# Optimization experiments

Hardware: AMD Instinct MI355X
Metric: run time of the kernel (lower is better)

Reference implementation:

```python
import jax, jax.numpy as jnp
import numpy as np

N, F, F_, H = 8192, 1024, 64, 4
LEAKY_ALPHA = 0.2
MASK_VAL = -1e10


def setup_inputs() -> dict:
    key = jax.random.key(0)
    k1, k2, k3, k4 = jax.random.split(key, 4)
    X = jax.random.normal(k1, (N, F), dtype=jnp.float32)
    # sparse-ish binary adjacency with self loops (A = A + I in the source script)
    A = (jax.random.uniform(k2, (N, N)) < 0.004).astype(jnp.float32)
    A = jnp.clip(A + jnp.eye(N, dtype=jnp.float32), 0.0, 1.0)
    W = jax.random.normal(k3, (H, F, F_), dtype=jnp.float32) * (1.0 / np.sqrt(F))
    attn_a = jax.random.normal(k4, (H, 2 * F_, 1), dtype=jnp.float32) * (1.0 / np.sqrt(2 * F_))
    bias = jnp.zeros((H, F_), dtype=jnp.float32)
    return {"X": X, "A": A, "W": W, "attn_a": attn_a, "bias": bias}


def reference(X, A, W, attn_a, bias):
    # features per head: [H, N, F_]
    feats = jnp.einsum('nf,hfk->hnk', X, W)
    # concat-score trick: [f_i, f_j] @ a == f_i @ a[:F_] + f_j @ a[F_:]
    a_self = attn_a[:, :F_, 0]   # [H, F_]
    a_neigh = attn_a[:, F_:, 0]  # [H, F_]
    s_self = jnp.einsum('hnk,hk->hn', feats, a_self)   # [H, N]
    s_neigh = jnp.einsum('hnk,hk->hn', feats, a_neigh)  # [H, N]
    scores = s_self[:, :, None] + s_neigh[:, None, :]   # [H, N, N]
    scores = jnp.where(scores > 0, scores, LEAKY_ALPHA * scores)  # LeakyReLU(0.2)
    scores = scores + MASK_VAL * (1.0 - A)[None]
    attn = jax.nn.softmax(scores, axis=-1)              # [H, N, N]
    # aggregate (dropout is identity at inference)
    out = jnp.einsum('hij,hjk->hik', attn, feats) + bias[:, None, :]  # [H, N, F_]
    out = jnp.transpose(out, (1, 0, 2)).reshape(X.shape[0], H * F_)   # concat heads
    return jax.nn.relu(out)
```

## Files before the change

kernel.cpp:

```cpp
#include <hip/hip_runtime.h>
#include <hip/hip_bf16.h>
#include <stdint.h>

#define NN 8192
#define FF 1024
#define FD 64
#define NH 4
#define CC 256
#define MAXE 192

typedef __attribute__((ext_vector_type(8))) short short8;
typedef __attribute__((ext_vector_type(4))) float f32x4;

__device__ __forceinline__ short bf16_rne(float f) {
    union { float f; uint32_t u; } v; v.f = f;
    uint32_t r = (v.u + 0x7FFFu + ((v.u >> 16) & 1u)) >> 16;
    return (short)(r & 0xFFFFu);
}

__global__ __launch_bounds__(256) void scan_kernel(const float* __restrict__ A,
                                                   int* __restrict__ nbr,
                                                   int* __restrict__ cnt) {
    __shared__ int idx[MAXE];
    __shared__ int c;
    const int row = blockIdx.x;
    const int t = threadIdx.x;
    if (t == 0) c = 0;
    __syncthreads();
    const f32x4* A4 = (const f32x4*)(A + (size_t)row * NN);
    for (int r = 0; r < 8; ++r) {
        int c4 = r * 256 + t;
        f32x4 v = __builtin_nontemporal_load(&A4[c4]);
        if (v.x > 0.5f) { int p = atomicAdd(&c, 1); if (p < MAXE) idx[p] = c4 * 4 + 0; }
        if (v.y > 0.5f) { int p = atomicAdd(&c, 1); if (p < MAXE) idx[p] = c4 * 4 + 1; }
        if (v.z > 0.5f) { int p = atomicAdd(&c, 1); if (p < MAXE) idx[p] = c4 * 4 + 2; }
        if (v.w > 0.5f) { int p = atomicAdd(&c, 1); if (p < MAXE) idx[p] = c4 * 4 + 3; }
    }
    __syncthreads();
    int n = min(c, MAXE);
    if (t < n) nbr[row * MAXE + t] = idx[t];
    if (t == 0) cnt[row] = n;
}

__global__ __launch_bounds__(256) void wt_kernel(const float* __restrict__ W,
                                                 short* __restrict__ Wt) {
    int gid = blockIdx.x * 256 + threadIdx.x;
    int k = gid & 1023;
    int n = (gid >> 10) & 63;
    int h = gid >> 16;
    Wt[gid] = bf16_rne(W[(h << 16) + k * 64 + n]);
}

__global__ __launch_bounds__(256) void xb_kernel(const float* __restrict__ X,
                                                 short* __restrict__ Xb) {
    int gid = blockIdx.x * 256 + threadIdx.x;
    float4 v = ((const float4*)X)[gid];
    short4 o;
    o.x = bf16_rne(v.x); o.y = bf16_rne(v.y);
    o.z = bf16_rne(v.z); o.w = bf16_rne(v.w);
    ((short4*)Xb)[gid] = o;
}

__global__ __launch_bounds__(256) void gemm_kernel(const short* __restrict__ Xb,
                                                   const short* __restrict__ Wt,
                                                   const float* __restrict__ attn_a,
                                                   float* __restrict__ feats,
                                                   float* __restrict__ s_self,
                                                   float* __restrict__ s_neigh) {
    __shared__ short Xs[64 * 40];
    __shared__ short Ws[64 * 40];
    const int h  = blockIdx.x;
    const int m0 = blockIdx.y * 64;
    const int t  = threadIdx.x;
    const int wave = t >> 6, lane = t & 63;
    const int q = lane >> 4, nl = lane & 15;
    const int srow = t >> 2, sk8 = (t & 3) * 8;

    f32x4 acc0 = {0.f,0.f,0.f,0.f}, acc1 = {0.f,0.f,0.f,0.f};
    f32x4 acc2 = {0.f,0.f,0.f,0.f}, acc3 = {0.f,0.f,0.f,0.f};

    const short* Xp = Xb + (size_t)(m0 + srow) * FF + sk8;
    const short* Wp = Wt + (size_t)(h * 64 + srow) * FF + sk8;

    for (int k0 = 0; k0 < FF; k0 += 32) {
        short8 xv = *(const short8*)(Xp + k0);
        short8 wv = *(const short8*)(Wp + k0);
        *(short8*)(&Xs[srow * 40 + sk8]) = xv;
        *(short8*)(&Ws[srow * 40 + sk8]) = wv;
        __syncthreads();
        short8 a  = *(const short8*)(&Xs[(wave * 16 + nl) * 40 + q * 8]);
        short8 b0 = *(const short8*)(&Ws[( 0 + nl) * 40 + q * 8]);
        short8 b1 = *(const short8*)(&Ws[(16 + nl) * 40 + q * 8]);
        short8 b2 = *(const short8*)(&Ws[(32 + nl) * 40 + q * 8]);
        short8 b3 = *(const short8*)(&Ws[(48 + nl) * 40 + q * 8]);
        acc0 = __builtin_amdgcn_mfma_f32_16x16x32_bf16(a, b0, acc0, 0, 0, 0);
        acc1 = __builtin_amdgcn_mfma_f32_16x16x32_bf16(a, b1, acc1, 0, 0, 0);
        acc2 = __builtin_amdgcn_mfma_f32_16x16x32_bf16(a, b2, acc2, 0, 0, 0);
        acc3 = __builtin_amdgcn_mfma_f32_16x16x32_bf16(a, b3, acc3, 0, 0, 0);
        __syncthreads();
    }
    const int row = m0 + wave * 16 + q * 4;
    const int colbase = h * 64 + nl;
    for (int r = 0; r < 4; ++r) {
        feats[(size_t)(row + r) * CC + colbase +  0] = acc0[r];
        feats[(size_t)(row + r) * CC + colbase + 16] = acc1[r];
        feats[(size_t)(row + r) * CC + colbase + 32] = acc2[r];
        feats[(size_t)(row + r) * CC + colbase + 48] = acc3[r];
    }
    const float A0 = attn_a[h * 128 + nl],      A1 = attn_a[h * 128 + nl + 16];
    const float A2 = attn_a[h * 128 + nl + 32], A3 = attn_a[h * 128 + nl + 48];
    const float B0 = attn_a[h * 128 + 64 + nl],      B1 = attn_a[h * 128 + 64 + nl + 16];
    const float B2 = attn_a[h * 128 + 64 + nl + 32], B3 = attn_a[h * 128 + 64 + nl + 48];
    for (int r = 0; r < 4; ++r) {
        float ps = acc0[r] * A0 + acc1[r] * A1 + acc2[r] * A2 + acc3[r] * A3;
        float pn = acc0[r] * B0 + acc1[r] * B1 + acc2[r] * B2 + acc3[r] * B3;
        for (int off = 1; off < 16; off <<= 1) {
            ps += __shfl_xor(ps, off);
            pn += __shfl_xor(pn, off);
        }
        if (nl == 0) {
            s_self [h * NN + row + r] = ps;
            s_neigh[h * NN + row + r] = pn;
        }
    }
}

__global__ __launch_bounds__(256) void smax_kernel(const int* __restrict__ nbr,
                                                   const int* __restrict__ cnt,
                                                   const float* __restrict__ feats,
                                                   const float* __restrict__ s_self,
                                                   const float* __restrict__ s_neigh,
                                                   const float* __restrict__ bias,
                                                   float* __restrict__ out) {
    __shared__ int js[MAXE];
    __shared__ float ps[NH][MAXE];
    const int row = blockIdx.x;
    const int t = threadIdx.x;
    const int h = t >> 6, lane = t & 63;
    const int n = cnt[row];
    if (t < n) js[t] = nbr[row * MAXE + t];
    __syncthreads();

    const float si = s_self[h * NN + row];
    const float* snh = s_neigh + h * NN;

    float m = -1e30f;
    for (int e = lane; e < n; e += 64) {
        float s = si + snh[js[e]];
        s = s > 0.f ? s : 0.2f * s;
        m = fmaxf(m, s);
    }
    for (int off = 1; off < 64; off <<= 1) m = fmaxf(m, __shfl_xor(m, off));

    float dsum = 0.f;
    for (int e = lane; e < n; e += 64) {
        float s = si + snh[js[e]];
        s = s > 0.f ? s : 0.2f * s;
        float p = __expf(s - m);
        ps[h][e] = p;
        dsum += p;
    }
    for (int off = 1; off < 64; off <<= 1) dsum += __shfl_xor(dsum, off);
    __syncthreads();

    float acc = 0.f;
    const float* fbase = feats + h * 64 + lane;
    #pragma unroll 4
    for (int e = 0; e < n; ++e) {
        acc = fmaf(ps[h][e], fbase[(size_t)js[e] * CC], acc);
    }
    float o = acc / dsum + bias[h * 64 + lane];
    out[(size_t)row * CC + h * 64 + lane] = fmaxf(o, 0.f);
}

extern "C" void kernel_launch(void* const* d_in, const int* in_sizes, int n_in,
                              void* d_out, int out_size, void* d_ws, size_t ws_size,
                              hipStream_t stream) {
    const float* X      = (const float*)d_in[0];
    const float* A      = (const float*)d_in[1];
    const float* W      = (const float*)d_in[2];
    const float* attn_a = (const float*)d_in[3];
    const float* bias   = (const float*)d_in[4];
    float* out = (float*)d_out;

    char* ws = (char*)d_ws;
    float* feats   = (float*)ws;
    float* s_self  = (float*)(ws + 8388608);
    float* s_neigh = (float*)(ws + 8519680);
    short* Wt      = (short*)(ws + 8650752);
    short* Xb      = (short*)(ws + 9175040);
    int*   nbr     = (int*)  (ws + 25952256);
    int*   cnt     = (int*)  (ws + 32243712);

    scan_kernel<<<NN, 256, 0, stream>>>(A, nbr, cnt);
    wt_kernel  <<<1024, 256, 0, stream>>>(W, Wt);
    xb_kernel  <<<8192, 256, 0, stream>>>(X, Xb);
    gemm_kernel<<<dim3(4, 128), 256, 0, stream>>>(Xb, Wt, attn_a, feats, s_self, s_neigh);
    smax_kernel<<<NN, 256, 0, stream>>>(nbr, cnt, feats, s_self, s_neigh, bias, out);
}
```

Baseline: 417.3 us.

## Store features as bf16 and parallelize neighbor aggregation across sub-waves

The GEMM now writes per-head features as bf16 instead of fp32, which halves the feature buffer and the bytes gathered per neighbor. The softmax kernel keeps the leaky-ReLU scores in registers so the second gather of s_neigh is skipped. Each wave now splits its neighbors across four 16-lane groups, each loading 4 bf16 values per neighbor, then combines the partial sums with shuffles. This removes the serial per-neighbor dependency chain and the block barrier before aggregation. The cost is bf16 rounding error in the aggregated features, and correctness now relies on ps being visible to other lanes of the same wave without a barrier.

```diff
diff --git a/kernel.cpp b/kernel.cpp
--- a/kernel.cpp
+++ b/kernel.cpp
@@ -10,12 +10,17 @@
 #define MAXE 192
 
 typedef __attribute__((ext_vector_type(8))) short short8;
+typedef __attribute__((ext_vector_type(4))) short short4v;
 typedef __attribute__((ext_vector_type(4))) float f32x4;
 
 __device__ __forceinline__ short bf16_rne(float f) {
     union { float f; uint32_t u; } v; v.f = f;
     uint32_t r = (v.u + 0x7FFFu + ((v.u >> 16) & 1u)) >> 16;
     return (short)(r & 0xFFFFu);
+}
+__device__ __forceinline__ float bf2f(short s) {
+    union { uint32_t u; float f; } v; v.u = ((uint32_t)(uint16_t)s) << 16;
+    return v.f;
 }
 
 __global__ __launch_bounds__(256) void scan_kernel(const float* __restrict__ A,
@@ -64,7 +69,7 @@
 __global__ __launch_bounds__(256) void gemm_kernel(const short* __restrict__ Xb,
                                                    const short* __restrict__ Wt,
                                                    const float* __restrict__ attn_a,
-                                                   float* __restrict__ feats,
+                                                   short* __restrict__ featb,
                                                    float* __restrict__ s_self,
                                                    float* __restrict__ s_neigh) {
     __shared__ short Xs[64 * 40];
@@ -102,10 +107,11 @@
     const int row = m0 + wave * 16 + q * 4;
     const int colbase = h * 64 + nl;
     for (int r = 0; r < 4; ++r) {
-        feats[(size_t)(row + r) * CC + colbase +  0] = acc0[r];
-        feats[(size_t)(row + r) * CC + colbase + 16] = acc1[r];
-        feats[(size_t)(row + r) * CC + colbase + 32] = acc2[r];
-        feats[(size_t)(row + r) * CC + colbase + 48] = acc3[r];
+        short* fr = featb + (size_t)(row + r) * CC + colbase;
+        fr[ 0] = bf16_rne(acc0[r]);
+        fr[16] = bf16_rne(acc1[r]);
+        fr[32] = bf16_rne(acc2[r]);
+        fr[48] = bf16_rne(acc3[r]);
     }
     const float A0 = attn_a[h * 128 + nl],      A1 = attn_a[h * 128 + nl + 16];
     const float A2 = attn_a[h * 128 + nl + 32], A3 = attn_a[h * 128 + nl + 48];
@@ -127,7 +133,7 @@
 
 __global__ __launch_bounds__(256) void smax_kernel(const int* __restrict__ nbr,
                                                    const int* __restrict__ cnt,
-                                                   const float* __restrict__ feats,
+                                                   const short* __restrict__ featb,
                                                    const float* __restrict__ s_self,
                                                    const float* __restrict__ s_neigh,
                                                    const float* __restrict__ bias,
@@ -144,33 +150,59 @@
     const float si = s_self[h * NN + row];
     const float* snh = s_neigh + h * NN;
 
-    float m = -1e30f;
-    for (int e = lane; e < n; e += 64) {
-        float s = si + snh[js[e]];
-        s = s > 0.f ? s : 0.2f * s;
-        m = fmaxf(m, s);
-    }
+    float sc[3];
+    #pragma unroll
+    for (int i = 0; i < 3; ++i) {
+        int e = lane + 64 * i;
+        float s = -1e30f;
+        if (e < n) {
+            s = si + snh[js[e]];
+            s = s > 0.f ? s : 0.2f * s;
+        }
+        sc[i] = s;
+    }
+    float m = fmaxf(sc[0], fmaxf(sc[1], sc[2]));
     for (int off = 1; off < 64; off <<= 1) m = fmaxf(m, __shfl_xor(m, off));
 
     float dsum = 0.f;
-    for (int e = lane; e < n; e += 64) {
-        float s = si + snh[js[e]];
-        s = s > 0.f ? s : 0.2f * s;
-        float p = __expf(s - m);
-        ps[h][e] = p;
-        dsum += p;
+    #pragma unroll
+    for (int i = 0; i < 3; ++i) {
+        int e = lane + 64 * i;
+        if (e < n) {
+            float p = __expf(sc[i] - m);
+            ps[h][e] = p;
+            dsum += p;
+        }
     }
     for (int off = 1; off < 64; off <<= 1) dsum += __shfl_xor(dsum, off);
-    __syncthreads();
-
-    float acc = 0.f;
-    const float* fbase = feats + h * 64 + lane;
-    #pragma unroll 4
-    for (int e = 0; e < n; ++e) {
-        acc = fmaf(ps[h][e], fbase[(size_t)js[e] * CC], acc);
-    }
-    float o = acc / dsum + bias[h * 64 + lane];
-    out[(size_t)row * CC + h * 64 + lane] = fmaxf(o, 0.f);
+
+    const int sub = lane >> 4;
+    const int l16 = lane & 15;
+    const short* fb = featb + h * 64 + l16 * 4;
+    f32x4 acc = {0.f, 0.f, 0.f, 0.f};
+    #pragma unroll 2
+    for (int e = sub; e < n; e += 4) {
+        int j = js[e];
+        float p = ps[h][e];
+        short4v f = *(const short4v*)(fb + (size_t)j * CC);
+        acc[0] = fmaf(p, bf2f(f.x), acc[0]);
+        acc[1] = fmaf(p, bf2f(f.y), acc[1]);
+        acc[2] = fmaf(p, bf2f(f.z), acc[2]);
+        acc[3] = fmaf(p, bf2f(f.w), acc[3]);
+    }
+    #pragma unroll
+    for (int k = 0; k < 4; ++k) {
+        acc[k] += __shfl_xor(acc[k], 16);
+        acc[k] += __shfl_xor(acc[k], 32);
+    }
+    if (sub == 0) {
+        float rd = 1.0f / dsum;
+        f32x4 o;
+        #pragma unroll
+        for (int k = 0; k < 4; ++k)
+            o[k] = fmaxf(acc[k] * rd + bias[h * 64 + l16 * 4 + k], 0.f);
+        *(f32x4*)(out + (size_t)row * CC + h * 64 + l16 * 4) = o;
+    }
 }
 
 extern "C" void kernel_launch(void* const* d_in, const int* in_sizes, int n_in,
@@ -184,17 +216,17 @@
     float* out = (float*)d_out;
 
     char* ws = (char*)d_ws;
-    float* feats   = (float*)ws;
-    float* s_self  = (float*)(ws + 8388608);
-    float* s_neigh = (float*)(ws + 8519680);
-    short* Wt      = (short*)(ws + 8650752);
-    short* Xb      = (short*)(ws + 9175040);
-    int*   nbr     = (int*)  (ws + 25952256);
-    int*   cnt     = (int*)  (ws + 32243712);
+    short* featb   = (short*)ws;
+    float* s_self  = (float*)(ws + 4194304);
+    float* s_neigh = (float*)(ws + 4325376);
+    short* Wt      = (short*)(ws + 4456448);
+    short* Xb      = (short*)(ws + 4980736);
+    int*   nbr     = (int*)  (ws + 21757952);
+    int*   cnt     = (int*)  (ws + 28049408);
 
     scan_kernel<<<NN, 256, 0, stream>>>(A, nbr, cnt);
     wt_kernel  <<<1024, 256, 0, stream>>>(W, Wt);
     xb_kernel  <<<8192, 256, 0, stream>>>(X, Xb);
-    gemm_kernel<<<dim3(4, 128), 256, 0, stream>>>(Xb, Wt, attn_a, feats, s_self, s_neigh);
-    smax_kernel<<<NN, 256, 0, stream>>>(nbr, cnt, feats, s_self, s_neigh, bias, out);
-}
+    gemm_kernel<<<dim3(4, 128), 256, 0, stream>>>(Xb, Wt, attn_a, featb, s_self, s_neigh);
+    smax_kernel<<<NN, 256, 0, stream>>>(nbr, cnt, featb, s_self, s_neigh, bias, out);
+}
```

After: 404.0 us. -3.2%, faster.
